# Kernel tuning notes

Measured on AMD Instinct MI355X. Metric: run time of the kernel, lower is better.

## Reference

```python
import jax, jax.numpy as jnp
import numpy as np

N = 100000
IN_C = 256
OUT_C = 64
E = 3200000


def _gcn_conv(x, src, dst, W, b, n_nodes):
    # Linear transform first (PyG GCNConv does lin then propagate)
    h = x @ W  # [N, out]
    # Symmetric normalization with self-loops already included in src/dst
    ones = jnp.ones(src.shape[0], dtype=h.dtype)
    deg = jax.ops.segment_sum(ones, dst, num_segments=n_nodes)  # in-degree incl self-loop
    dinv = jnp.where(deg > 0, jax.lax.rsqrt(deg), 0.0)
    norm = dinv[src] * dinv[dst]  # [E+N]
    msg = h[src] * norm[:, None]  # gather + scale
    out = jax.ops.segment_sum(msg, dst, num_segments=n_nodes)  # scatter-add
    return out + b


def setup_inputs() -> dict:
    key = jax.random.key(0)
    k1, k2, k3, k4, k5, k6 = jax.random.split(key, 6)
    x = jax.random.normal(k1, (N, IN_C), dtype=jnp.float32)
    edge_index = jax.random.randint(k2, (2, E), 0, N, dtype=jnp.int64)
    s = 1.0 / np.sqrt(IN_C)
    W_mu = jax.random.uniform(k3, (IN_C, OUT_C), jnp.float32, -s, s)
    b_mu = jnp.zeros((OUT_C,), jnp.float32)
    W_ls = jax.random.uniform(k4, (IN_C, OUT_C), jnp.float32, -s, s)
    b_ls = jnp.zeros((OUT_C,), jnp.float32)
    return {"x": x, "edge_index": edge_index, "W_mu": W_mu, "b_mu": b_mu, "W_ls": W_ls, "b_ls": b_ls}


def reference(x, edge_index, W_mu, b_mu, W_ls, b_ls):
    n_nodes = x.shape[0]
    loops = jnp.arange(n_nodes, dtype=edge_index.dtype)
    src = jnp.concatenate([edge_index[0], loops])  # add self-loops
    dst = jnp.concatenate([edge_index[1], loops])
    mu = _gcn_conv(x, src, dst, W_mu, b_mu, n_nodes)
    logstd = _gcn_conv(x, src, dst, W_ls, b_ls, n_nodes)
    return (mu, logstd)
```

## Files before the change

kernel.cpp:

```cpp
#include <hip/hip_runtime.h>
#include <hip/hip_bf16.h>


#define IN_C 256
#define HC   128
#define OC   64

__global__ void k_detect(const void* ei, int n_scan, long long nn, int* flag) {
    __shared__ int bad;
    if (threadIdx.x == 0) bad = 0;
    __syncthreads();
    const long long* p = (const long long*)ei;
    for (int i = threadIdx.x; i < n_scan; i += blockDim.x) {
        long long v = p[i];
        if (v < 0 || v >= nn) bad = 1;
    }
    __syncthreads();
    if (threadIdx.x == 0) *flag = bad;
}

__global__ __launch_bounds__(256) void k_zero(int* cnt, int* cursor, int n) {
    int i = blockIdx.x * 256 + threadIdx.x;
    if (i < n) { cnt[i] = 0; cursor[i] = 0; }
}

__global__ __launch_bounds__(256) void k_count(const void* ei, int* cnt, int E, const int* flag) {
    int e0 = (blockIdx.x * 256 + threadIdx.x) * 4;
    if (e0 >= E) return;
    if (e0 + 3 < E) {
        int d[4];
        if (*flag) {
            int4 v = *(const int4*)((const int*)ei + (size_t)E + e0);
            d[0] = v.x; d[1] = v.y; d[2] = v.z; d[3] = v.w;
        } else {
            const long long* p = (const long long*)ei + (size_t)E + e0;
            longlong2 a = *(const longlong2*)p;
            longlong2 b = *(const longlong2*)(p + 2);
            d[0] = (int)a.x; d[1] = (int)a.y; d[2] = (int)b.x; d[3] = (int)b.y;
        }
        #pragma unroll
        for (int u = 0; u < 4; ++u) atomicAdd(&cnt[d[u]], 1);
    } else {
        for (int e = e0; e < E; ++e) {
            int d = (*flag) ? ((const int*)ei)[(size_t)E + e]
                            : (int)((const long long*)ei)[(size_t)E + e];
            atomicAdd(&cnt[d], 1);
        }
    }
}

__global__ void k_scan(const int* __restrict__ cnt, int* __restrict__ rowptr, int n) {
    __shared__ int part[1024];
    const int tid = threadIdx.x;
    const int per = (n + 1023) >> 10;
    const int lo  = tid * per;
    const int hi  = min(lo + per, n);
    int s = 0;
    for (int i = lo; i < hi; ++i) s += cnt[i];
    part[tid] = s;
    __syncthreads();
    for (int off = 1; off < 1024; off <<= 1) {
        int v = (tid >= off) ? part[tid - off] : 0;
        __syncthreads();
        part[tid] += v;
        __syncthreads();
    }
    int run = (tid > 0) ? part[tid - 1] : 0;
    for (int i = lo; i < hi; ++i) { rowptr[i] = run; run += cnt[i]; }
    if (hi == n) rowptr[n] = run;
}

__global__ __launch_bounds__(256) void k_dinv(const int* __restrict__ cnt, float* dinv, int n) {
    int i = blockIdx.x * 256 + threadIdx.x;
    if (i < n) dinv[i] = rsqrtf((float)(cnt[i] + 1));
}

__global__ __launch_bounds__(256) void k_fill(const void* ei, const int* __restrict__ rowptr,
                                              int* cursor, int* __restrict__ esrc,
                                              int E, const int* flag) {
    int e0 = (blockIdx.x * 256 + threadIdx.x) * 4;
    if (e0 >= E) return;
    if (e0 + 3 < E) {
        int s[4], d[4];
        if (*flag) {
            int4 vs = *(const int4*)((const int*)ei + e0);
            int4 vd = *(const int4*)((const int*)ei + (size_t)E + e0);
            s[0] = vs.x; s[1] = vs.y; s[2] = vs.z; s[3] = vs.w;
            d[0] = vd.x; d[1] = vd.y; d[2] = vd.z; d[3] = vd.w;
        } else {
            const long long* ps = (const long long*)ei + e0;
            const long long* pd = (const long long*)ei + (size_t)E + e0;
            longlong2 a = *(const longlong2*)ps;
            longlong2 b = *(const longlong2*)(ps + 2);
            longlong2 c = *(const longlong2*)pd;
            longlong2 g = *(const longlong2*)(pd + 2);
            s[0] = (int)a.x; s[1] = (int)a.y; s[2] = (int)b.x; s[3] = (int)b.y;
            d[0] = (int)c.x; d[1] = (int)c.y; d[2] = (int)g.x; d[3] = (int)g.y;
        }
        #pragma unroll
        for (int u = 0; u < 4; ++u) {
            int pos = rowptr[d[u]] + atomicAdd(&cursor[d[u]], 1);
            esrc[pos] = s[u];
        }
    } else {
        for (int e = e0; e < E; ++e) {
            int s, d;
            if (*flag) {
                s = ((const int*)ei)[e]; d = ((const int*)ei)[(size_t)E + e];
            } else {
                s = (int)((const long long*)ei)[e]; d = (int)((const long long*)ei)[(size_t)E + e];
            }
            int pos = rowptr[d] + atomicAdd(&cursor[d], 1);
            esrc[pos] = s;
        }
    }
}

#define BR 64
#define KC 32
__global__ __launch_bounds__(256) void k_gemm(const float* __restrict__ x,
                                              const float* __restrict__ Wmu,
                                              const float* __restrict__ Wls,
                                              float* __restrict__ hout, int nrows) {
    __shared__ float xs[BR][KC + 4];
    __shared__ float wsm[KC][HC];
    const int tid  = threadIdx.x;
    const int trow = tid >> 4;
    const int tcol = tid & 15;
    const int r0   = trow * 4;
    const int c0   = tcol * 4;
    const size_t rowbase = (size_t)blockIdx.x * BR;

    float acc[4][8];
    #pragma unroll
    for (int i = 0; i < 4; ++i)
        #pragma unroll
        for (int j = 0; j < 8; ++j) acc[i][j] = 0.0f;

    for (int kc = 0; kc < IN_C; kc += KC) {
        __syncthreads();
        {
            int lr = tid >> 3, lk = (tid & 7) * 4;
            #pragma unroll
            for (int half = 0; half < 2; ++half) {
                size_t gr = rowbase + lr + half * 32;
                float4 v = make_float4(0.f, 0.f, 0.f, 0.f);
                if (gr < (size_t)nrows)
                    v = *(const float4*)(x + gr * IN_C + kc + lk);
                *(float4*)&xs[lr + half * 32][lk] = v;
            }
        }
        #pragma unroll
        for (int i = 0; i < 4; ++i) {
            int q  = tid + 256 * i;
            int k  = q >> 5;
            int cq = (q & 31) * 4;
            const float* srcw = (cq < OC) ? (Wmu + (size_t)(kc + k) * OC + cq)
                                          : (Wls + (size_t)(kc + k) * OC + (cq - OC));
            *(float4*)&wsm[k][cq] = *(const float4*)srcw;
        }
        __syncthreads();

        #pragma unroll 8
        for (int k = 0; k < KC; ++k) {
            float4 w0 = *(const float4*)&wsm[k][c0];
            float4 w1 = *(const float4*)&wsm[k][c0 + OC];
            float xv[4];
            #pragma unroll
            for (int i = 0; i < 4; ++i) xv[i] = xs[r0 + i][k];
            #pragma unroll
            for (int i = 0; i < 4; ++i) {
                acc[i][0] += xv[i] * w0.x; acc[i][1] += xv[i] * w0.y;
                acc[i][2] += xv[i] * w0.z; acc[i][3] += xv[i] * w0.w;
                acc[i][4] += xv[i] * w1.x; acc[i][5] += xv[i] * w1.y;
                acc[i][6] += xv[i] * w1.z; acc[i][7] += xv[i] * w1.w;
            }
        }
    }
    #pragma unroll
    for (int i = 0; i < 4; ++i) {
        size_t gr = rowbase + r0 + i;
        if (gr < (size_t)nrows) {
            *(float4*)(hout + gr * HC + c0)      = make_float4(acc[i][0], acc[i][1], acc[i][2], acc[i][3]);
            *(float4*)(hout + gr * HC + OC + c0) = make_float4(acc[i][4], acc[i][5], acc[i][6], acc[i][7]);
        }
    }
}

__global__ __launch_bounds__(256) void k_out(const float* __restrict__ h,
                                             const int* __restrict__ rowptr,
                                             const int* __restrict__ esrc,
                                             const float* __restrict__ dinv,
                                             const float* __restrict__ bmu,
                                             const float* __restrict__ bls,
                                             float* __restrict__ out_mu,
                                             float* __restrict__ out_ls, int n) {
    int node = blockIdx.x * 4 + (threadIdx.x >> 6);
    if (node >= n) return;
    int lane = threadIdx.x & 63;
    const float2* __restrict__ h2 = (const float2*)h;

    float di = dinv[node];
    float2 self = h2[(size_t)node * 64 + lane];
    float w  = di * di;
    float ax = self.x * w, ay = self.y * w;

    int k   = rowptr[node];
    int end = rowptr[node + 1];

    for (; k + 7 < end; k += 8) {
        int   s[8];
        float nm[8];
        float2 v[8];
        #pragma unroll
        for (int u = 0; u < 8; ++u) s[u] = esrc[k + u];
        #pragma unroll
        for (int u = 0; u < 8; ++u) nm[u] = dinv[s[u]] * di;
        #pragma unroll
        for (int u = 0; u < 8; ++u) v[u] = h2[(size_t)s[u] * 64 + lane];
        #pragma unroll
        for (int u = 0; u < 8; ++u) { ax += v[u].x * nm[u]; ay += v[u].y * nm[u]; }
    }
    for (; k < end; ++k) {
        int s0 = esrc[k];
        float n0 = dinv[s0] * di;
        float2 v0 = h2[(size_t)s0 * 64 + lane];
        ax += v0.x * n0;
        ay += v0.y * n0;
    }

    if (lane < 32) {
        float2 b = ((const float2*)bmu)[lane];
        ((float2*)out_mu)[(size_t)node * 32 + lane] = make_float2(ax + b.x, ay + b.y);
    } else {
        float2 b = ((const float2*)bls)[lane - 32];
        ((float2*)out_ls)[(size_t)node * 32 + (lane - 32)] = make_float2(ax + b.x, ay + b.y);
    }
}

extern "C" void kernel_launch(void* const* d_in, const int* in_sizes, int n_in,
                              void* d_out, int out_size, void* d_ws, size_t ws_size,
                              hipStream_t stream) {
    const float* x   = (const float*)d_in[0];
    const void*  ei  = d_in[1];
    const float* Wmu = (const float*)d_in[2];
    const float* bmu = (const float*)d_in[3];
    const float* Wls = (const float*)d_in[4];
    const float* bls = (const float*)d_in[5];

    const int N = in_sizes[0] / IN_C;
    const int E = in_sizes[1] / 2;

    float* out_mu = (float*)d_out;
    float* out_ls = (float*)d_out + (size_t)N * OC;

    char* w = (char*)d_ws;
    auto align256 = [](size_t v) { return (v + 255) & ~(size_t)255; };
    int*   flag   = (int*)w;                  size_t off = 256;
    int*   cnt    = (int*)(w + off);          off += align256((size_t)N * 4);
    int*   cursor = (int*)(w + off);          off += align256((size_t)N * 4);
    float* dinv   = (float*)(w + off);        off += align256((size_t)N * 4);
    int*   rowptr = (int*)(w + off);          off += align256((size_t)(N + 1) * 4);
    int*   esrc   = (int*)(w + off);          off += align256((size_t)E * 4);
    float* h      = (float*)(w + off);        off += align256((size_t)N * HC * 4);

    int n_scan = E < 4096 ? E : 4096;
    hipLaunchKernelGGL(k_detect, dim3(1), dim3(256), 0, stream, ei, n_scan, (long long)N, flag);

    int gN = (N + 255) / 256;
    hipLaunchKernelGGL(k_zero, dim3(gN), dim3(256), 0, stream, cnt, cursor, N);

    int gE4 = (E + 1023) / 1024;
    hipLaunchKernelGGL(k_count, dim3(gE4), dim3(256), 0, stream, ei, cnt, E, flag);

    hipLaunchKernelGGL(k_scan, dim3(1), dim3(1024), 0, stream, cnt, rowptr, N);
    hipLaunchKernelGGL(k_dinv, dim3(gN), dim3(256), 0, stream, cnt, dinv, N);
    hipLaunchKernelGGL(k_fill, dim3(gE4), dim3(256), 0, stream, ei, rowptr, cursor, esrc, E, flag);

    int gG = (N + BR - 1) / BR;
    hipLaunchKernelGGL(k_gemm, dim3(gG), dim3(256), 0, stream, x, Wmu, Wls, h, N);

    int gO = (N + 3) / 4;
    hipLaunchKernelGGL(k_out, dim3(gO), dim3(256), 0, stream, h, rowptr, esrc, dinv, bmu, bls, out_mu, out_ls, N);
}
```

Before: 921.5 us.

## Use split-bf16 MFMA for the feature transform GEMM

Replaces the scalar FP32 tiled GEMM that computes x@[W_mu|W_ls] with a matrix-core version. Each FP32 operand is split into high and low bf16 parts, and three MFMA 16x16x32 products are accumulated to recover near-FP32 accuracy. The row tile grows to 128 rows per block, and the conversion to bf16 happens while staging tiles into shared memory. The aim is to cut the ALU-bound GEMM time, at the cost of extra conversion work and weight reloading per block, plus slightly reduced precision.

```diff
diff --git a/kernel.cpp b/kernel.cpp
--- a/kernel.cpp
+++ b/kernel.cpp
@@ -5,6 +5,19 @@
 #define IN_C 256
 #define HC   128
 #define OC   64
+
+typedef __attribute__((ext_vector_type(8))) short bf16x8;
+typedef __attribute__((ext_vector_type(4))) float f32x4;
+
+__device__ __forceinline__ short f2bf(float f) {
+    union { float f; unsigned u; } v; v.f = f;
+    unsigned r = v.u + 0x7fffu + ((v.u >> 16) & 1u);
+    return (short)(r >> 16);
+}
+__device__ __forceinline__ float bf2f(short s) {
+    union { float f; unsigned u; } v; v.u = ((unsigned)(unsigned short)s) << 16;
+    return v.f;
+}
 
 __global__ void k_detect(const void* ei, int n_scan, long long nn, int* flag) {
     __shared__ int bad;
@@ -116,75 +129,93 @@
     }
 }
 
-#define BR 64
-#define KC 32
+#define GP 40
 __global__ __launch_bounds__(256) void k_gemm(const float* __restrict__ x,
                                               const float* __restrict__ Wmu,
                                               const float* __restrict__ Wls,
                                               float* __restrict__ hout, int nrows) {
-    __shared__ float xs[BR][KC + 4];
-    __shared__ float wsm[KC][HC];
+    __shared__ short Ah[128][GP], Al[128][GP];
+    __shared__ short Bh[128][GP], Bl[128][GP];
     const int tid  = threadIdx.x;
-    const int trow = tid >> 4;
-    const int tcol = tid & 15;
-    const int r0   = trow * 4;
-    const int c0   = tcol * 4;
-    const size_t rowbase = (size_t)blockIdx.x * BR;
-
-    float acc[4][8];
+    const int wid  = tid >> 6;
+    const int lane = tid & 63;
+    const int l15  = lane & 15;
+    const int k0   = (lane >> 4) * 8;
+    const size_t rowbase = (size_t)blockIdx.x * 128;
+
+    f32x4 acc[2][8];
     #pragma unroll
-    for (int i = 0; i < 4; ++i)
-        #pragma unroll
-        for (int j = 0; j < 8; ++j) acc[i][j] = 0.0f;
-
-    for (int kc = 0; kc < IN_C; kc += KC) {
+    for (int rt = 0; rt < 2; ++rt)
+        #pragma unroll
+        for (int ct = 0; ct < 8; ++ct) acc[rt][ct] = (f32x4){0.f, 0.f, 0.f, 0.f};
+
+    for (int kc = 0; kc < IN_C; kc += 32) {
         __syncthreads();
-        {
-            int lr = tid >> 3, lk = (tid & 7) * 4;
+        #pragma unroll
+        for (int it = 0; it < 4; ++it) {
+            int q = tid + 256 * it;
+            int r = q >> 3, f = q & 7;
+            size_t gr = rowbase + r;
+            float4 v = make_float4(0.f, 0.f, 0.f, 0.f);
+            if (gr < (size_t)nrows)
+                v = *(const float4*)(x + gr * IN_C + kc + f * 4);
+            short h0 = f2bf(v.x), h1 = f2bf(v.y), h2 = f2bf(v.z), h3 = f2bf(v.w);
+            short l0 = f2bf(v.x - bf2f(h0)), l1 = f2bf(v.y - bf2f(h1));
+            short l2 = f2bf(v.z - bf2f(h2)), l3 = f2bf(v.w - bf2f(h3));
+            *(ushort4*)&Ah[r][f * 4] = make_ushort4((unsigned short)h0, (unsigned short)h1,
+                                                    (unsigned short)h2, (unsigned short)h3);
+            *(ushort4*)&Al[r][f * 4] = make_ushort4((unsigned short)l0, (unsigned short)l1,
+                                                    (unsigned short)l2, (unsigned short)l3);
+        }
+        #pragma unroll
+        for (int it = 0; it < 2; ++it) {
+            int q = tid + 256 * it;
+            int c = q >> 2, g = q & 3;
+            const float* wc = (c < OC) ? (Wmu + c) : (Wls + (c - OC));
+            short hb[8], lb[8];
             #pragma unroll
-            for (int half = 0; half < 2; ++half) {
-                size_t gr = rowbase + lr + half * 32;
-                float4 v = make_float4(0.f, 0.f, 0.f, 0.f);
-                if (gr < (size_t)nrows)
-                    v = *(const float4*)(x + gr * IN_C + kc + lk);
-                *(float4*)&xs[lr + half * 32][lk] = v;
+            for (int j = 0; j < 8; ++j) {
+                float v = wc[(size_t)(kc + g * 8 + j) * OC];
+                short h = f2bf(v);
+                hb[j] = h;
+                lb[j] = f2bf(v - bf2f(h));
             }
-        }
-        #pragma unroll
-        for (int i = 0; i < 4; ++i) {
-            int q  = tid + 256 * i;
-            int k  = q >> 5;
-            int cq = (q & 31) * 4;
-            const float* srcw = (cq < OC) ? (Wmu + (size_t)(kc + k) * OC + cq)
-                                          : (Wls + (size_t)(kc + k) * OC + (cq - OC));
-            *(float4*)&wsm[k][cq] = *(const float4*)srcw;
+            *(bf16x8*)&Bh[c][g * 8] = *(bf16x8*)hb;
+            *(bf16x8*)&Bl[c][g * 8] = *(bf16x8*)lb;
         }
         __syncthreads();
 
-        #pragma unroll 8
-        for (int k = 0; k < KC; ++k) {
-            float4 w0 = *(const float4*)&wsm[k][c0];
-            float4 w1 = *(const float4*)&wsm[k][c0 + OC];
-            float xv[4];
+        bf16x8 ah[2], al[2];
+        #pragma unroll
+        for (int rt = 0; rt < 2; ++rt) {
+            int r = rt * 64 + wid * 16 + l15;
+            ah[rt] = *(bf16x8*)&Ah[r][k0];
+            al[rt] = *(bf16x8*)&Al[r][k0];
+        }
+        #pragma unroll
+        for (int ct = 0; ct < 8; ++ct) {
+            bf16x8 bh = *(bf16x8*)&Bh[ct * 16 + l15][k0];
+            bf16x8 bl = *(bf16x8*)&Bl[ct * 16 + l15][k0];
             #pragma unroll
-            for (int i = 0; i < 4; ++i) xv[i] = xs[r0 + i][k];
+            for (int rt = 0; rt < 2; ++rt) {
+                acc[rt][ct] = __builtin_amdgcn_mfma_f32_16x16x32_bf16(al[rt], bh, acc[rt][ct], 0, 0, 0);
+                acc[rt][ct] = __builtin_amdgcn_mfma_f32_16x16x32_bf16(ah[rt], bl, acc[rt][ct], 0, 0, 0);
+                acc[rt][ct] = __builtin_amdgcn_mfma_f32_16x16x32_bf16(ah[rt], bh, acc[rt][ct], 0, 0, 0);
+            }
+        }
+    }
+
+    const int orow = (lane >> 4) * 4;
+    #pragma unroll
+    for (int rt = 0; rt < 2; ++rt)
+        #pragma unroll
+        for (int ct = 0; ct < 8; ++ct)
             #pragma unroll
-            for (int i = 0; i < 4; ++i) {
-                acc[i][0] += xv[i] * w0.x; acc[i][1] += xv[i] * w0.y;
-                acc[i][2] += xv[i] * w0.z; acc[i][3] += xv[i] * w0.w;
-                acc[i][4] += xv[i] * w1.x; acc[i][5] += xv[i] * w1.y;
-                acc[i][6] += xv[i] * w1.z; acc[i][7] += xv[i] * w1.w;
+            for (int rg = 0; rg < 4; ++rg) {
+                size_t grow = rowbase + rt * 64 + wid * 16 + orow + rg;
+                if (grow < (size_t)nrows)
+                    hout[grow * HC + ct * 16 + l15] = acc[rt][ct][rg];
             }
-        }
-    }
-    #pragma unroll
-    for (int i = 0; i < 4; ++i) {
-        size_t gr = rowbase + r0 + i;
-        if (gr < (size_t)nrows) {
-            *(float4*)(hout + gr * HC + c0)      = make_float4(acc[i][0], acc[i][1], acc[i][2], acc[i][3]);
-            *(float4*)(hout + gr * HC + OC + c0) = make_float4(acc[i][4], acc[i][5], acc[i][6], acc[i][7]);
-        }
-    }
 }
 
 __global__ __launch_bounds__(256) void k_out(const float* __restrict__ h,
@@ -277,7 +308,7 @@
     hipLaunchKernelGGL(k_dinv, dim3(gN), dim3(256), 0, stream, cnt, dinv, N);
     hipLaunchKernelGGL(k_fill, dim3(gE4), dim3(256), 0, stream, ei, rowptr, cursor, esrc, E, flag);
 
-    int gG = (N + BR - 1) / BR;
+    int gG = (N + 127) / 128;
     hipLaunchKernelGGL(k_gemm, dim3(gG), dim3(256), 0, stream, x, Wmu, Wls, h, N);
 
     int gO = (N + 3) / 4;
```

Result: no change. 908.6 us (-1.4%).
